# Kernel tuning notes

Hardware: AMD Instinct MI355X
Metric: run time of the kernel (lower is better)

## Reference

```python
import jax, jax.numpy as jnp
import numpy as np

N, T = 1024, 32
D_FEAT, GATE_START, GATE_END = 158, 158, 221
D_MODEL = 256
T_NHEAD, S_NHEAD = 4, 2
BETA = 5.0
LN_EPS = 1e-5


def _ln(x, g, b):
    mu = jnp.mean(x, axis=-1, keepdims=True)
    var = jnp.mean(jnp.square(x - mu), axis=-1, keepdims=True)
    return (x - mu) * jax.lax.rsqrt(var + LN_EPS) * g + b


def _pos_enc(t, d):
    pos = jnp.arange(t, dtype=jnp.float32)[:, None]
    div = jnp.exp(jnp.arange(0, d, 2, dtype=jnp.float32) * (-np.log(10000.0) / d))
    pe = jnp.zeros((t, d), dtype=jnp.float32)
    pe = pe.at[:, 0::2].set(jnp.sin(pos * div))
    pe = pe.at[:, 1::2].set(jnp.cos(pos * div))
    return pe


def _mha(xn, qw, kw, vw, nhead, temperature):
    # xn: [B, S, D] (already layer-normed); attention over axis S
    B, S, D = xn.shape
    dh = D // nhead
    q = (xn @ qw.T).reshape(B, S, nhead, dh)
    k = (xn @ kw.T).reshape(B, S, nhead, dh)
    v = (xn @ vw.T).reshape(B, S, nhead, dh)
    scores = jnp.einsum('bshd,bthd->bhst', q, k) / temperature
    a = jax.nn.softmax(scores, axis=-1)
    return jnp.einsum('bhst,bthd->bshd', a, v).reshape(B, S, D)


def _block(x, qw, kw, vw, n1g, n1b, n2g, n2b, f1w, f1b, f2w, f2b, nhead, temperature):
    xn = _ln(x, n1g, n1b)
    xt = xn + _mha(xn, qw, kw, vw, nhead, temperature)
    xt = _ln(xt, n2g, n2b)
    ffn = jnp.maximum(xt @ f1w.T + f1b, 0.0) @ f2w.T + f2b
    return xt + ffn


def _forward(x, gate_w, gate_b, proj_w, proj_b,
             tq, tk, tv, tn1g, tn1b, tn2g, tn2b, tf1w, tf1b, tf2w, tf2b,
             sq, sk, sv, sn1g, sn1b, sn2g, sn2b, sf1w, sf1b, sf2w, sf2b,
             temp_w, out_w, out_b):
    src = x[:, :, :GATE_START]                     # [N, T, d_feat]
    gate_in = x[:, -1, GATE_START:GATE_END]        # [N, d_gate]
    gate = D_FEAT * jax.nn.softmax((gate_in @ gate_w.T + gate_b) / BETA, axis=-1)
    src = src * gate[:, None, :]
    z = src @ proj_w.T + proj_b                    # [N, T, d_model]
    z = z + _pos_enc(z.shape[1], D_MODEL)
    # TAttention: attend over time, unscaled scores (temperature=1)
    z = _block(z, tq, tk, tv, tn1g, tn1b, tn2g, tn2b, tf1w, tf1b, tf2w, tf2b,
               T_NHEAD, 1.0)
    # SAttention: attend over stocks, temperature = sqrt(d_model/nhead)
    zs = _block(z.swapaxes(0, 1), sq, sk, sv, sn1g, sn1b, sn2g, sn2b,
                sf1w, sf1b, sf2w, sf2b, S_NHEAD, float(np.sqrt(D_MODEL / S_NHEAD)))
    z = zs.swapaxes(0, 1)                          # [N, T, d_model]
    # TemporalAttention pooling
    h = z @ temp_w.T
    lam = jax.nn.softmax(jnp.einsum('ntd,nd->nt', h, h[:, -1, :]), axis=1)
    pooled = jnp.einsum('nt,ntd->nd', lam, z)
    return (pooled @ out_w.T + out_b).squeeze(-1)  # [N]


def setup_inputs() -> dict:
    key = jax.random.key(0)
    ks = iter(jax.random.split(key, 32))
    s = 0.02
    d, f, g = D_MODEL, D_FEAT, GATE_END - GATE_START
    inp = {
        'x': jax.random.normal(next(ks), (N, T, GATE_END), dtype=jnp.float32),
        'gate_w': jax.random.normal(next(ks), (f, g)) * s,
        'gate_b': jnp.zeros((f,)),
        'proj_w': jax.random.normal(next(ks), (d, f)) * s,
        'proj_b': jnp.zeros((d,)),
        'tq': jax.random.normal(next(ks), (d, d)) * s,
        'tk': jax.random.normal(next(ks), (d, d)) * s,
        'tv': jax.random.normal(next(ks), (d, d)) * s,
        'tn1g': jnp.ones((d,)), 'tn1b': jnp.zeros((d,)),
        'tn2g': jnp.ones((d,)), 'tn2b': jnp.zeros((d,)),
        'tf1w': jax.random.normal(next(ks), (d, d)) * s, 'tf1b': jnp.zeros((d,)),
        'tf2w': jax.random.normal(next(ks), (d, d)) * s, 'tf2b': jnp.zeros((d,)),
        'sq': jax.random.normal(next(ks), (d, d)) * s,
        'sk': jax.random.normal(next(ks), (d, d)) * s,
        'sv': jax.random.normal(next(ks), (d, d)) * s,
        'sn1g': jnp.ones((d,)), 'sn1b': jnp.zeros((d,)),
        'sn2g': jnp.ones((d,)), 'sn2b': jnp.zeros((d,)),
        'sf1w': jax.random.normal(next(ks), (d, d)) * s, 'sf1b': jnp.zeros((d,)),
        'sf2w': jax.random.normal(next(ks), (d, d)) * s, 'sf2b': jnp.zeros((d,)),
        'temp_w': jax.random.normal(next(ks), (d, d)) * s,
        'out_w': jax.random.normal(next(ks), (1, d)) * s,
        'out_b': jnp.zeros((1,)),
    }
    return {k: v.astype(jnp.float32) for k, v in inp.items()}


def reference(x, gate_w, gate_b, proj_w, proj_b,
              tq, tk, tv, tn1g, tn1b, tn2g, tn2b, tf1w, tf1b, tf2w, tf2b,
              sq, sk, sv, sn1g, sn1b, sn2g, sn2b, sf1w, sf1b, sf2w, sf2b,
              temp_w, out_w, out_b):
    return _forward(x, gate_w, gate_b, proj_w, proj_b,
                    tq, tk, tv, tn1g, tn1b, tn2g, tn2b, tf1w, tf1b, tf2w, tf2b,
                    sq, sk, sv, sn1g, sn1b, sn2g, sn2b, sf1w, sf1b, sf2w, sf2b,
                    temp_w, out_w, out_b)
```

## Files before the change

### kernel.cpp

```cpp
#include <hip/hip_runtime.h>
#include <math.h>

#define NB   1024
#define TSEQ 32
#define DM   256
#define DF   158
#define GDIM 63
#define XROW 221

typedef unsigned short u16;
typedef __attribute__((ext_vector_type(8))) __bf16 bf16x8;
typedef __attribute__((ext_vector_type(4))) float f32x4;
#define MFMA16(a,b,c) __builtin_amdgcn_mfma_f32_16x16x32_bf16(a,b,c,0,0,0)

#define MODE_PROJ 0
#define MODE_QKVT 1
#define MODE_QKVS 2
#define MODE_TEMP 3

__device__ __forceinline__ u16 f2bf(float f){
  union { float f; unsigned int u; } c; c.f = f;
  unsigned int u = c.u;
  u += 0x7fffu + ((u >> 16) & 1u);
  return (u16)(u >> 16);
}

__device__ __forceinline__ u16 f2bf_t(float f){
  union { float f; unsigned int u; } c; c.f = f;
  return (u16)(c.u >> 16);
}

__device__ __forceinline__ void gl2lds16(const u16* g, u16* lds_wave_base, int lane){
#if __has_builtin(__builtin_amdgcn_global_load_lds)
  __builtin_amdgcn_global_load_lds(
      (const __attribute__((address_space(1))) unsigned int*)g,
      (__attribute__((address_space(3))) unsigned int*)lds_wave_base,
      16, 0, 0);
#else
  *reinterpret_cast<uint4*>(lds_wave_base + lane * 8) =
      *reinterpret_cast<const uint4*>(g);
#endif
}

__device__ __forceinline__ void ln_rows32(float* buf, int stride,
                                          const float* __restrict__ g,
                                          const float* __restrict__ b,
                                          int tid)
{
  const int s = tid >> 3, j = tid & 7;
  float* row = buf + s * stride;
  float sum = 0.f, sq = 0.f;
  #pragma unroll
  for (int k = 0; k < DM; k += 8){
    float v = row[k + j];
    sum += v; sq += v * v;
  }
  #pragma unroll
  for (int o = 1; o < 8; o <<= 1){
    sum += __shfl_xor(sum, o);
    sq  += __shfl_xor(sq, o);
  }
  const float mu  = sum * (1.f / DM);
  const float var = sq * (1.f / DM) - mu * mu;
  const float rs  = rsqrtf(var + 1e-5f);
  #pragma unroll
  for (int k = 0; k < DM; k += 8){
    float v = row[k + j];
    row[k + j] = (v - mu) * rs * g[k + j] + b[k + j];
  }
}

#define WB_TOT 770048

__global__ __launch_bounds__(256) void kConvAll(
    const float* __restrict__ tq, const float* __restrict__ tk, const float* __restrict__ tv,
    const float* __restrict__ sq, const float* __restrict__ sk, const float* __restrict__ sv,
    const float* __restrict__ tf1, const float* __restrict__ tf2,
    const float* __restrict__ sf1, const float* __restrict__ sf2,
    const float* __restrict__ tw, const float* __restrict__ pw,
    u16* __restrict__ WB)
{
  int i = blockIdx.x * 256 + threadIdx.x;
  if (i >= WB_TOT) return;
  if (i < 720896){
    int j = i >> 16, o = i & 65535;
    const float* s;
    switch (j){
      case 0: s = tq; break;  case 1: s = tk; break;  case 2: s = tv; break;
      case 3: s = sq; break;  case 4: s = sk; break;  case 5: s = sv; break;
      case 6: s = tf1; break; case 7: s = tf2; break;
      case 8: s = sf1; break; case 9: s = sf2; break;
      default: s = tw; break;
    }
    WB[i] = f2bf(s[o]);
  } else {
    int k = i - 720896;
    int row = k / 192, col = k - row * 192;
    WB[i] = (col < DF) ? f2bf(pw[row * DF + col]) : (u16)0;
  }
}


__global__ __launch_bounds__(256) void kGateSrc(
    const float* __restrict__ x,
    const float* __restrict__ gate_w, const float* __restrict__ gate_b,
    u16* __restrict__ SRC)
{
  __shared__ float s_gate[DF];
  __shared__ float s_gi[GDIM];
  const int tid = threadIdx.x;
  const int n = blockIdx.x;

  if (tid < GDIM) s_gi[tid] = x[(n * TSEQ + (TSEQ - 1)) * XROW + DF + tid];
  __syncthreads();
  float logit = 0.f;
  if (tid < DF){
    logit = gate_b[tid];
    const float* __restrict__ wr = gate_w + tid * GDIM;
    for (int g = 0; g < GDIM; ++g) logit += s_gi[g] * wr[g];
    logit *= 0.2f;
    s_gate[tid] = logit;
  }
  __syncthreads();
  {
    float mx = -1e30f;
    for (int f = 0; f < DF; ++f) mx = fmaxf(mx, s_gate[f]);
    float sm = 0.f;
    for (int f = 0; f < DF; ++f) sm += __expf(s_gate[f] - mx);
    __syncthreads();
    if (tid < DF) s_gate[tid] = (float)DF * __expf(logit - mx) / sm;
  }
  __syncthreads();

  for (int e = tid; e < TSEQ * 192; e += 256){
    int t = e / 192, f = e - t * 192;
    float v = 0.f;
    if (f < DF) v = x[(n * TSEQ + t) * XROW + f] * s_gate[f];
    SRC[(size_t)(n * TSEQ + t) * 192 + f] = f2bf(v);
  }
}


__global__ __launch_bounds__(256) void gemm_bf16(
    const u16* __restrict__ A, const u16* __restrict__ B,
    const int K, const int mode,
    const float* __restrict__ bias,
    float* __restrict__ outf,
    u16* __restrict__ ob0, u16* __restrict__ ob1, u16* __restrict__ ob2)
{
  __shared__ alignas(16) u16 sA[128 * 64];
  __shared__ alignas(16) u16 sB[128 * 64];
  const int tid = threadIdx.x;
  const int wv = tid >> 6, lane = tid & 63;
  const int wr = wv >> 1, wc = wv & 1;
  const int quad = lane >> 4, lc = lane & 15;
  const int n0 = blockIdx.y * 128;
  const bool tmaj = (mode == MODE_QKVS);
  const int tt = tmaj ? (blockIdx.x & 31) : 0;
  const int nb = tmaj ? (blockIdx.x >> 5) : 0;
  const int m0 = tmaj ? 0 : blockIdx.x * 128;

  f32x4 acc[4][4];
  #pragma unroll
  for (int i = 0; i < 4; ++i)
    #pragma unroll
    for (int j = 0; j < 4; ++j) acc[i][j] = (f32x4){0.f,0.f,0.f,0.f};

  for (int kt = 0; kt < K; kt += 64){
    __syncthreads();
    #pragma unroll
    for (int j = 0; j < 4; ++j){
      int c = wv * 64 + lane + j * 256;
      int row = c >> 3, blk = c & 7;
      int arow = tmaj ? ((nb * 128 + row) * 32 + tt) : (m0 + row);
      gl2lds16(A + (size_t)arow * K + kt + ((blk ^ (row & 7)) * 8),
               &sA[(wv * 64 + j * 256) * 8], lane);
      gl2lds16(B + (size_t)(n0 + row) * K + kt + ((blk ^ (row & 7)) * 8),
               &sB[(wv * 64 + j * 256) * 8], lane);
    }
    __syncthreads();
    #pragma unroll
    for (int kc = 0; kc < 2; ++kc){
      const int sw = ((kc * 4 + quad) ^ (lc & 7)) * 8;
      bf16x8 a[4], b[4];
      #pragma unroll
      for (int i = 0; i < 4; ++i){
        a[i] = *reinterpret_cast<const bf16x8*>(&sA[(wr * 64 + i * 16 + lc) * 64 + sw]);
        b[i] = *reinterpret_cast<const bf16x8*>(&sB[(wc * 64 + i * 16 + lc) * 64 + sw]);
      }
      #pragma unroll
      for (int i = 0; i < 4; ++i)
        #pragma unroll
        for (int j = 0; j < 4; ++j)
          acc[i][j] = MFMA16(a[i], b[j], acc[i][j]);
    }
  }

  const int rb = wr * 64 + quad * 4;
  const int cb = wc * 64 + lc;

  if (mode == MODE_PROJ){
    #pragma unroll
    for (int i = 0; i < 4; ++i)
      #pragma unroll
      for (int r = 0; r < 4; ++r){
        int row = m0 + rb + i * 16 + r;
        float ft = (float)(row & 31);
        #pragma unroll
        for (int j = 0; j < 4; ++j){
          int col = n0 + cb + j * 16;
          float div = __expf((float)(col & ~1) * -0.035977892f);
          float ang = ft * div;
          float pe = (col & 1) ? __cosf(ang) : __sinf(ang);
          outf[(size_t)row * 256 + col] = acc[i][j][r] + bias[col] + pe;
        }
      }
  } else if (mode == MODE_QKVT){
    #pragma unroll
    for (int i = 0; i < 4; ++i)
      #pragma unroll
      for (int r = 0; r < 4; ++r){
        int row = m0 + rb + i * 16 + r;
        #pragma unroll
        for (int j = 0; j < 4; ++j){
          int col = n0 + cb + j * 16;
          int sel = col >> 8, c = col & 255;
          u16 v = f2bf(acc[i][j][r]);
          if (sel == 0)      ob0[(size_t)row * 256 + c] = v;
          else if (sel == 1) ob1[(size_t)row * 256 + c] = v;
          else {
            int h = c >> 6, dd = c & 63;
            ob2[(((size_t)(row >> 5) * 4 + h) * 64 + dd) * 32 + (row & 31)] = v;
          }
        }
      }
  } else if (mode == MODE_QKVS){
    #pragma unroll
    for (int i = 0; i < 4; ++i)
      #pragma unroll
      for (int r = 0; r < 4; ++r){
        int rl = rb + i * 16 + r;
        int n = nb * 128 + rl;
        #pragma unroll
        for (int j = 0; j < 4; ++j){
          int col = n0 + cb + j * 16;
          int sel = col >> 8, c = col & 255;
          u16 v = f2bf(acc[i][j][r]);
          if (sel == 0)      ob0[((size_t)tt * NB + n) * 256 + c] = v;
          else if (sel == 1) ob1[((size_t)tt * NB + n) * 256 + c] = v;
          else {
            int h = c >> 7, dd = c & 127;
            ob2[(((size_t)tt * 2 + h) * 128 + dd) * NB + n] = v;
          }
        }
      }
  } else {
    #pragma unroll
    for (int i = 0; i < 4; ++i)
      #pragma unroll
      for (int r = 0; r < 4; ++r){
        int row = m0 + rb + i * 16 + r;
        #pragma unroll
        for (int j = 0; j < 4; ++j){
          int col = n0 + cb + j * 16;
          outf[(size_t)row * 256 + col] = acc[i][j][r];
        }
      }
  }
}


__global__ __launch_bounds__(256) void kLN(
    const float* __restrict__ X, const float* __restrict__ g,
    const float* __restrict__ b,
    u16* __restrict__ Xb, float* __restrict__ Xf)
{
  __shared__ float s_z[32 * DM];
  const int tid = threadIdx.x;
  const size_t base = (size_t)blockIdx.x * (32 * DM);
  for (int e = tid; e < 32 * DM; e += 256) s_z[e] = X[base + e];
  __syncthreads();
  ln_rows32(s_z, DM, g, b, tid);
  __syncthreads();
  for (int e = tid; e < 32 * DM; e += 256){
    float v = s_z[e];
    Xb[base + e] = f2bf(v);
    Xf[base + e] = v;
  }
}


__global__ __launch_bounds__(512) void kFFN(
    const float* __restrict__ X,
    const float* __restrict__ lg, const float* __restrict__ lb,
    const u16* __restrict__ w1, const float* __restrict__ b1,
    const u16* __restrict__ w2, const float* __restrict__ b2,
    float* __restrict__ outf, u16* __restrict__ obdual)
{
  __shared__ alignas(16) u16 sAB[24576];
  __shared__ alignas(16) u16 s_h1[128 * 256];
  __shared__ float s_mu[128], s_rs[128];
  __shared__ float s_lg[256], s_lb[256], s_b1[256], s_b2[256];

  const int tid = threadIdx.x;
  const int wv = tid >> 6, lane = tid & 63;
  const int quad = lane >> 4, lc = lane & 15;
  const int m0 = blockIdx.x * 128;
  const int m0w = (wv >> 1) * 32;
  const int n0w = (wv & 1) * 128;
  u16* sA = sAB;
  u16* sB = sAB + 8192;

  if (tid < 256){
    s_lg[tid] = lg[tid]; s_lb[tid] = lb[tid];
    s_b1[tid] = b1[tid]; s_b2[tid] = b2[tid];
  }

  {
    const int row = tid >> 2, j = tid & 3;
    const float4* xr = reinterpret_cast<const float4*>(X + (size_t)(m0 + row) * 256);
    float sum = 0.f, sq = 0.f;
    #pragma unroll
    for (int k = 0; k < 16; ++k){
      float4 v = xr[j + 4 * k];
      sum += v.x + v.y + v.z + v.w;
      sq  += v.x*v.x + v.y*v.y + v.z*v.z + v.w*v.w;
    }
    sum += __shfl_xor(sum, 1); sq += __shfl_xor(sq, 1);
    sum += __shfl_xor(sum, 2); sq += __shfl_xor(sq, 2);
    if (j == 0){
      float mu = sum * (1.f / 256.f);
      s_mu[row] = mu;
      s_rs[row] = rsqrtf(sq * (1.f / 256.f) - mu * mu + 1e-5f);
    }
  }
  __syncthreads();

  f32x4 acc[2][8];
  #pragma unroll
  for (int mt = 0; mt < 2; ++mt)
    #pragma unroll
    for (int j = 0; j < 8; ++j) acc[mt][j] = (f32x4){0.f,0.f,0.f,0.f};

  for (int kt = 0; kt < 4; ++kt){
    __syncthreads();
    {
      const int row = tid >> 2, c0 = (tid & 3) * 16;
      const float mu = s_mu[row], rs = s_rs[row];
      const float* xp = X + (size_t)(m0 + row) * 256 + kt * 64 + c0;
      u16 v16[16];
      #pragma unroll
      for (int k = 0; k < 4; ++k){
        float4 v = *reinterpret_cast<const float4*>(xp + 4 * k);
        int col = kt * 64 + c0 + 4 * k;
        v16[4*k+0] = f2bf((v.x - mu) * rs * s_lg[col+0] + s_lb[col+0]);
        v16[4*k+1] = f2bf((v.y - mu) * rs * s_lg[col+1] + s_lb[col+1]);
        v16[4*k+2] = f2bf((v.z - mu) * rs * s_lg[col+2] + s_lb[col+2]);
        v16[4*k+3] = f2bf((v.w - mu) * rs * s_lg[col+3] + s_lb[col+3]);
      }
      int b0 = c0 >> 3;
      *reinterpret_cast<uint4*>(&sA[row * 64 + ((b0    ) ^ (row & 7)) * 8]) = *reinterpret_cast<uint4*>(&v16[0]);
      *reinterpret_cast<uint4*>(&sA[row * 64 + ((b0 + 1) ^ (row & 7)) * 8]) = *reinterpret_cast<uint4*>(&v16[8]);
    }
    #pragma unroll
    for (int i = 0; i < 4; ++i){
      int c = tid + i * 512;
      int row = c >> 3, blk = c & 7;
      *reinterpret_cast<uint4*>(&sB[row * 64 + (blk ^ (row & 7)) * 8]) =
        *reinterpret_cast<const uint4*>(w1 + (size_t)row * 256 + kt * 64 + blk * 8);
    }
    __syncthreads();
    #pragma unroll
    for (int kc = 0; kc < 2; ++kc){
      const int sw = ((kc * 4 + quad) ^ (lc & 7)) * 8;
      bf16x8 a[2], b[8];
      #pragma unroll
      for (int mt = 0; mt < 2; ++mt)
        a[mt] = *reinterpret_cast<const bf16x8*>(&sA[(m0w + mt * 16 + lc) * 64 + sw]);
      #pragma unroll
      for (int j = 0; j < 8; ++j)
        b[j] = *reinterpret_cast<const bf16x8*>(&sB[(n0w + j * 16 + lc) * 64 + sw]);
      #pragma unroll
      for (int mt = 0; mt < 2; ++mt)
        #pragma unroll
        for (int j = 0; j < 8; ++j)
          acc[mt][j] = MFMA16(a[mt], b[j], acc[mt][j]);
    }
  }
  __syncthreads();

  #pragma unroll
  for (int mt = 0; mt < 2; ++mt)
    #pragma unroll
    for (int r = 0; r < 4; ++r){
      int row = m0w + mt * 16 + quad * 4 + r;
      #pragma unroll
      for (int j = 0; j < 8; ++j){
        int col = n0w + j * 16 + lc;
        u16 v = f2bf(fmaxf(acc[mt][j][r] + s_b1[col], 0.f));
        s_h1[row * 256 + (((col >> 3) ^ (row & 31)) << 3) + (col & 7)] = v;
      }
    }

  #pragma unroll
  for (int mt = 0; mt < 2; ++mt)
    #pragma unroll
    for (int j = 0; j < 8; ++j) acc[mt][j] = (f32x4){0.f,0.f,0.f,0.f};

  for (int kt = 0; kt < 4; ++kt){
    __syncthreads();
    #pragma unroll
    for (int i = 0; i < 4; ++i){
      int c = tid + i * 512;
      int row = c >> 3, blk = c & 7;
      *reinterpret_cast<uint4*>(&sAB[row * 64 + (blk ^ (row & 7)) * 8]) =
        *reinterpret_cast<const uint4*>(w2 + (size_t)row * 256 + kt * 64 + blk * 8);
    }
    __syncthreads();
    #pragma unroll
    for (int kc = 0; kc < 2; ++kc){
      const int sw = ((kc * 4 + quad) ^ (lc & 7)) * 8;
      bf16x8 a[2], b[8];
      #pragma unroll
      for (int mt = 0; mt < 2; ++mt){
        int row = m0w + mt * 16 + lc;
        int cb = kt * 8 + kc * 4 + quad;
        a[mt] = *reinterpret_cast<const bf16x8*>(
            &s_h1[row * 256 + ((cb ^ (row & 31)) << 3)]);
      }
      #pragma unroll
      for (int j = 0; j < 8; ++j)
        b[j] = *reinterpret_cast<const bf16x8*>(&sAB[(n0w + j * 16 + lc) * 64 + sw]);
      #pragma unroll
      for (int mt = 0; mt < 2; ++mt)
        #pragma unroll
        for (int j = 0; j < 8; ++j)
          acc[mt][j] = MFMA16(a[mt], b[j], acc[mt][j]);
    }
  }

  #pragma unroll
  for (int mt = 0; mt < 2; ++mt)
    #pragma unroll
    for (int r = 0; r < 4; ++r){
      int rowl = m0w + mt * 16 + quad * 4 + r;
      const float mu = s_mu[rowl], rs = s_rs[rowl];
      size_t base = (size_t)(m0 + rowl) * 256;
      #pragma unroll
      for (int j = 0; j < 8; ++j){
        int col = n0w + j * 16 + lc;
        float xn = (X[base + col] - mu) * rs * s_lg[col] + s_lb[col];
        float v = acc[mt][j][r] + s_b2[col] + xn;
        outf[base + col] = v;
        if (obdual) obdual[base + col] = f2bf(v);
      }
    }
}


__global__ __launch_bounds__(256) void kAttnT(
    const u16* __restrict__ Qt, const u16* __restrict__ Kt,
    const u16* __restrict__ VtT, const float* __restrict__ XN1f,
    float* __restrict__ X2)
{
  __shared__ alignas(16) u16 sQ[4][32 * 72];
  __shared__ alignas(16) u16 sK[4][32 * 72];
  __shared__ alignas(16) u16 sV[4][64 * 40];
  __shared__ alignas(16) u16 sP[4][32 * 40];

  const int tid = threadIdx.x;
  const int wv = tid >> 6, lane = tid & 63;
  const int quad = lane >> 4, lc = lane & 15;
  const int n = blockIdx.x;
  const int h = wv;
  const f32x4 zero4 = {0.f, 0.f, 0.f, 0.f};

  #pragma unroll
  for (int i = 0; i < 4; ++i){
    int c = lane + 64 * i;
    int row = c >> 3, blk = c & 7;
    *reinterpret_cast<uint4*>(&sQ[wv][row * 72 + blk * 8]) =
      *reinterpret_cast<const uint4*>(&Qt[((size_t)n * 32 + row) * 256 + h * 64 + blk * 8]);
    *reinterpret_cast<uint4*>(&sK[wv][row * 72 + blk * 8]) =
      *reinterpret_cast<const uint4*>(&Kt[((size_t)n * 32 + row) * 256 + h * 64 + blk * 8]);
    int rv = c >> 2, bv = c & 3;
    *reinterpret_cast<uint4*>(&sV[wv][rv * 40 + bv * 8]) =
      *reinterpret_cast<const uint4*>(&VtT[(((size_t)n * 4 + h) * 64 + rv) * 32 + bv * 8]);
  }
  __syncthreads();

  f32x4 s[2][2];
  #pragma unroll
  for (int mt = 0; mt < 2; ++mt)
    #pragma unroll
    for (int ct = 0; ct < 2; ++ct) s[mt][ct] = zero4;
  #pragma unroll
  for (int kc = 0; kc < 2; ++kc){
    bf16x8 aq[2], bk[2];
    #pragma unroll
    for (int mt = 0; mt < 2; ++mt)
      aq[mt] = *reinterpret_cast<const bf16x8*>(&sQ[wv][(mt * 16 + lc) * 72 + kc * 32 + quad * 8]);
    #pragma unroll
    for (int ct = 0; ct < 2; ++ct)
      bk[ct] = *reinterpret_cast<const bf16x8*>(&sK[wv][(ct * 16 + lc) * 72 + kc * 32 + quad * 8]);
    #pragma unroll
    for (int mt = 0; mt < 2; ++mt)
      #pragma unroll
      for (int ct = 0; ct < 2; ++ct)
        s[mt][ct] = MFMA16(aq[mt], bk[ct], s[mt][ct]);
  }

  #pragma unroll
  for (int mt = 0; mt < 2; ++mt){
    #pragma unroll
    for (int r = 0; r < 4; ++r){
      float v0 = s[mt][0][r], v1 = s[mt][1][r];
      float mx = fmaxf(v0, v1);
      #pragma unroll
      for (int msk = 1; msk < 16; msk <<= 1) mx = fmaxf(mx, __shfl_xor(mx, msk));
      float p0 = __expf(v0 - mx), p1 = __expf(v1 - mx);
      float sm = p0 + p1;
      #pragma unroll
      for (int msk = 1; msk < 16; msk <<= 1) sm += __shfl_xor(sm, msk);
      float inv = 1.f / sm;
      sP[wv][(mt * 16 + quad * 4 + r) * 40 + lc]      = f2bf(p0 * inv);
      sP[wv][(mt * 16 + quad * 4 + r) * 40 + lc + 16] = f2bf(p1 * inv);
    }
  }
  __syncthreads();

  #pragma unroll
  for (int mt = 0; mt < 2; ++mt){
    bf16x8 ap = *reinterpret_cast<const bf16x8*>(&sP[wv][(mt * 16 + lc) * 40 + quad * 8]);
    #pragma unroll
    for (int ct = 0; ct < 4; ++ct){
      bf16x8 bv = *reinterpret_cast<const bf16x8*>(&sV[wv][(ct * 16 + lc) * 40 + quad * 8]);
      f32x4 o = MFMA16(ap, bv, zero4);
      #pragma unroll
      for (int r = 0; r < 4; ++r){
        int t = mt * 16 + quad * 4 + r;
        size_t idx = ((size_t)n * 32 + t) * 256 + h * 64 + ct * 16 + lc;
        X2[idx] = XN1f[idx] + o[r];
      }
    }
  }
}


__global__ __launch_bounds__(512) void kB2_flash_mfma(
    const u16* __restrict__ Qh, const u16* __restrict__ Kh,
    const u16* __restrict__ VT, const float* __restrict__ XNs,
    float* __restrict__ XT)
{
  __shared__ alignas(16) u16 smem[28160];
  u16* s_k  = smem;
  u16* s_vt = smem + 8704;
  u16* s_p  = smem + 17920;

  const int tid = threadIdx.x;
  const int wv = tid >> 6, lane = tid & 63;
  const int wq = wv & 3, wk = wv >> 2;
  const int quad = lane >> 4, lc = lane & 15;
  const int t = blockIdx.x >> 1, h = blockIdx.x & 1;
  const int n0 = blockIdx.y * 128;
  const float c_exp2 = 0.12752887f;
  const int qb = n0 + wq * 32;

  bf16x8 qf[2][4];
  #pragma unroll
  for (int mt = 0; mt < 2; ++mt){
    const u16* qp = Qh + ((size_t)(t * NB + qb + mt * 16 + lc)) * DM + h * 128 + quad * 8;
    #pragma unroll
    for (int kc = 0; kc < 4; ++kc)
      qf[mt][kc] = *reinterpret_cast<const bf16x8*>(qp + kc * 32);
  }

  f32x4 o[2][8];
  #pragma unroll
  for (int mt = 0; mt < 2; ++mt)
    #pragma unroll
    for (int f = 0; f < 8; ++f) o[mt][f] = (f32x4){0.f, 0.f, 0.f, 0.f};
  float l_acc[2][4] = {{0.f,0.f,0.f,0.f},{0.f,0.f,0.f,0.f}};

  const u16* kbase  = Kh + (size_t)t * NB * DM + h * 128;
  const u16* vtbase = VT + (size_t)(t * 2 + h) * 128 * NB;
  u16* pw = s_p + wv * 1280;

  for (int j0 = 0; j0 < NB; j0 += 64){
    __syncthreads();
    #pragma unroll
    for (int it = 0; it < 2; ++it){
      int c = tid + it * 512;
      int row = c >> 4, part = c & 15;
      *reinterpret_cast<uint4*>(&s_k[row * 136 + part * 8]) =
        *reinterpret_cast<const uint4*>(kbase + (size_t)(j0 + row) * DM + part * 8);
      int rv = c >> 3, pv = c & 7;
      *reinterpret_cast<uint4*>(&s_vt[rv * 72 + pv * 8]) =
        *reinterpret_cast<const uint4*>(vtbase + (size_t)rv * NB + j0 + pv * 8);
    }
    __syncthreads();

    f32x4 s[2][2];
    #pragma unroll
    for (int mt = 0; mt < 2; ++mt)
      #pragma unroll
      for (int nt = 0; nt < 2; ++nt) s[mt][nt] = (f32x4){0.f,0.f,0.f,0.f};
    #pragma unroll
    for (int kc = 0; kc < 4; ++kc){
      #pragma unroll
      for (int nt = 0; nt < 2; ++nt){
        bf16x8 bk = *reinterpret_cast<const bf16x8*>(
            &s_k[(lc + 16 * nt + 32 * wk) * 136 + kc * 32 + quad * 8]);
        #pragma unroll
        for (int mt = 0; mt < 2; ++mt)
          s[mt][nt] = MFMA16(qf[mt][kc], bk, s[mt][nt]);
      }
    }

    #pragma unroll
    for (int mt = 0; mt < 2; ++mt)
      #pragma unroll
      for (int nt = 0; nt < 2; ++nt)
        #pragma unroll
        for (int r = 0; r < 4; ++r){
          float p = exp2f(s[mt][nt][r] * c_exp2);
          l_acc[mt][r] += p;
          pw[(mt * 16 + quad * 4 + r) * 40 + lc + 16 * nt] = f2bf_t(p);
        }

    bf16x8 ap[2];
    #pragma unroll
    for (int mt = 0; mt < 2; ++mt)
      ap[mt] = *reinterpret_cast<const bf16x8*>(&pw[(mt * 16 + lc) * 40 + quad * 8]);
    #pragma unroll
    for (int f = 0; f < 8; ++f){
      bf16x8 bv = *reinterpret_cast<const bf16x8*>(
          &s_vt[(lc + 16 * f) * 72 + 32 * wk + quad * 8]);
      #pragma unroll
      for (int mt = 0; mt < 2; ++mt)
        o[mt][f] = MFMA16(ap[mt], bv, o[mt][f]);
    }
  }

  float* fo = (float*)smem;
  float* fl = (float*)smem + 8192;

  __syncthreads();
  if (wk == 1){
    int base = (wq * 64 + lane) * 32;
    #pragma unroll
    for (int f = 0; f < 8; ++f)
      #pragma unroll
      for (int r = 0; r < 4; ++r) fo[base + f * 4 + r] = o[0][f][r];
    int lb = (wq * 64 + lane) * 8;
    #pragma unroll
    for (int mt = 0; mt < 2; ++mt)
      #pragma unroll
      for (int r = 0; r < 4; ++r) fl[lb + mt * 4 + r] = l_acc[mt][r];
  }
  __syncthreads();
  if (wk == 0){
    int base = (wq * 64 + lane) * 32;
    #pragma unroll
    for (int f = 0; f < 8; ++f)
      #pragma unroll
      for (int r = 0; r < 4; ++r) o[0][f][r] += fo[base + f * 4 + r];
    int lb = (wq * 64 + lane) * 8;
    #pragma unroll
    for (int mt = 0; mt < 2; ++mt)
      #pragma unroll
      for (int r = 0; r < 4; ++r){
        l_acc[mt][r] += fl[lb + mt * 4 + r];
        #pragma unroll
        for (int msk = 1; msk < 16; msk <<= 1)
          l_acc[mt][r] += __shfl_xor(l_acc[mt][r], msk);
      }
    #pragma unroll
    for (int r = 0; r < 4; ++r){
      float linv = 1.f / l_acc[0][r];
      int row = qb + quad * 4 + r;
      size_t xnb = ((size_t)row * TSEQ + t) * DM + h * 128 + lc;
      size_t xtb = ((size_t)t * NB + row) * DM + h * 128 + lc;
      #pragma unroll
      for (int f = 0; f < 8; ++f)
        XT[xtb + f * 16] = XNs[xnb + f * 16] + o[0][f][r] * linv;
    }
  }
  __syncthreads();
  if (wk == 1){
    int base = (wq * 64 + lane) * 32;
    #pragma unroll
    for (int f = 0; f < 8; ++f)
      #pragma unroll
      for (int r = 0; r < 4; ++r) fo[base + f * 4 + r] = o[1][f][r];
  }
  __syncthreads();
  if (wk == 0){
    int base = (wq * 64 + lane) * 32;
    #pragma unroll
    for (int f = 0; f < 8; ++f)
      #pragma unroll
      for (int r = 0; r < 4; ++r) o[1][f][r] += fo[base + f * 4 + r];
    #pragma unroll
    for (int r = 0; r < 4; ++r){
      float linv = 1.f / l_acc[1][r];
      int row = qb + 16 + quad * 4 + r;
      size_t xnb = ((size_t)row * TSEQ + t) * DM + h * 128 + lc;
      size_t xtb = ((size_t)t * NB + row) * DM + h * 128 + lc;
      #pragma unroll
      for (int f = 0; f < 8; ++f)
        XT[xtb + f * 16] = XNs[xnb + f * 16] + o[1][f][r] * linv;
    }
  }
}


__global__ __launch_bounds__(256) void kC_pool(
    const float* __restrict__ Ht, const float* __restrict__ ZS,
    const float* __restrict__ out_w, const float* __restrict__ out_b,
    float* __restrict__ out)
{
  __shared__ float s_z[32 * DM];
  __shared__ float s_h[32 * 260];
  __shared__ float s_sc[32];
  __shared__ float s_red[4];
  const int tid = threadIdx.x;
  const int n = blockIdx.x;

  for (int e = tid; e < 32 * DM; e += 256){
    int i = e >> 8, dd = e & 255;
    s_h[i * 260 + dd] = Ht[((size_t)i * NB + n) * DM + dd];
    s_z[e]            = ZS[((size_t)i * NB + n) * DM + dd];
  }
  __syncthreads();

  {
    const int s = tid >> 3, j = tid & 7;
    float acc = 0.f;
    #pragma unroll
    for (int k = 0; k < DM; k += 8) acc += s_h[s * 260 + k + j] * s_h[31 * 260 + k + j];
    #pragma unroll
    for (int o = 1; o < 8; o <<= 1) acc += __shfl_xor(acc, o);
    if (j == 0) s_sc[s] = acc;
  }
  __syncthreads();

  float mx = -1e30f;
  #pragma unroll
  for (int s = 0; s < 32; ++s) mx = fmaxf(mx, s_sc[s]);
  float sm = 0.f;
  #pragma unroll
  for (int s = 0; s < 32; ++s) sm += __expf(s_sc[s] - mx);
  const float inv = 1.f / sm;

  const int d = tid;
  float pooled = 0.f;
  #pragma unroll
  for (int s = 0; s < 32; ++s) pooled += __expf(s_sc[s] - mx) * inv * s_z[s * DM + d];

  float val = pooled * out_w[d];
  #pragma unroll
  for (int o = 1; o < 64; o <<= 1) val += __shfl_xor(val, o);
  if ((tid & 63) == 0) s_red[tid >> 6] = val;
  __syncthreads();
  if (tid == 0) out[n] = s_red[0] + s_red[1] + s_red[2] + s_red[3] + out_b[0];
}


extern "C" void kernel_launch(void* const* d_in, const int* in_sizes, int n_in,
                              void* d_out, int out_size, void* d_ws, size_t ws_size,
                              hipStream_t stream)
{
  const float* x      = (const float*)d_in[0];
  const float* gate_w = (const float*)d_in[1];
  const float* gate_b = (const float*)d_in[2];
  const float* proj_w = (const float*)d_in[3];
  const float* proj_b = (const float*)d_in[4];
  const float* tq   = (const float*)d_in[5];
  const float* tk   = (const float*)d_in[6];
  const float* tv   = (const float*)d_in[7];
  const float* tn1g = (const float*)d_in[8];
  const float* tn1b = (const float*)d_in[9];
  const float* tn2g = (const float*)d_in[10];
  const float* tn2b = (const float*)d_in[11];
  const float* tf1w = (const float*)d_in[12];
  const float* tf1b = (const float*)d_in[13];
  const float* tf2w = (const float*)d_in[14];
  const float* tf2b = (const float*)d_in[15];
  const float* sq   = (const float*)d_in[16];
  const float* sk   = (const float*)d_in[17];
  const float* sv   = (const float*)d_in[18];
  const float* sn1g = (const float*)d_in[19];
  const float* sn1b = (const float*)d_in[20];
  const float* sn2g = (const float*)d_in[21];
  const float* sn2b = (const float*)d_in[22];
  const float* sf1w = (const float*)d_in[23];
  const float* sf1b = (const float*)d_in[24];
  const float* sf2w = (const float*)d_in[25];
  const float* sf2b = (const float*)d_in[26];
  const float* temp_w = (const float*)d_in[27];
  const float* out_w  = (const float*)d_in[28];
  const float* out_b  = (const float*)d_in[29];

  float* W = (float*)d_ws;
  const size_t F = (size_t)NB * TSEQ * DM;

  float* Z  = W;
  float* XF = W + F;
  u16* U0 = (u16*)(W + 2 * F);
  u16* U1 = (u16*)(W + 2 * F) + F;
  u16* U2 = (u16*)(W + 3 * F);
  u16* U3 = (u16*)(W + 3 * F) + F;
  u16* SRC = (u16*)(W + 4 * F);
  u16* WB  = (u16*)(W + 4 * F + 3145728 + 4096);

  kConvAll<<<(WB_TOT + 255) / 256, 256, 0, stream>>>(
      tq, tk, tv, sq, sk, sv, tf1w, tf2w, sf1w, sf2w, temp_w, proj_w, WB);
  kGateSrc<<<NB, 256, 0, stream>>>(x, gate_w, gate_b, SRC);
  gemm_bf16<<<dim3(256, 2), 256, 0, stream>>>(SRC, WB + 720896, 192, MODE_PROJ,
      proj_b, Z, nullptr, nullptr, nullptr);
  kLN<<<NB, 256, 0, stream>>>(Z, tn1g, tn1b, U0, XF);
  gemm_bf16<<<dim3(256, 6), 256, 0, stream>>>(U0, WB, 256, MODE_QKVT,
      nullptr, nullptr, U1, U2, U3);
  kAttnT<<<NB, 256, 0, stream>>>(U1, U2, U3, XF, Z);
  kFFN<<<256, 512, 0, stream>>>(Z, tn2g, tn2b, WB + 393216, tf1b,
      WB + 458752, tf2b, Z, nullptr);
  kLN<<<NB, 256, 0, stream>>>(Z, sn1g, sn1b, U2, XF);
  gemm_bf16<<<dim3(256, 6), 256, 0, stream>>>(U2, WB + 196608, 256, MODE_QKVS,
      nullptr, nullptr, U3, U1, U0);
  kB2_flash_mfma<<<dim3(64, 8), 512, 0, stream>>>(U3, U1, U0, XF, Z);
  kFFN<<<256, 512, 0, stream>>>(Z, sn2g, sn2b, WB + 524288, sf1b,
      WB + 589824, sf2b, Z, U0);
  gemm_bf16<<<dim3(256, 2), 256, 0, stream>>>(U0, WB + 655360, 256, MODE_TEMP,
      nullptr, XF, nullptr, nullptr, nullptr);
  kC_pool<<<NB, 256, 0, stream>>>(XF, Z, out_w, out_b, (float*)d_out);
}
```

Before: 478.8 us.

## Widen GEMM tiles to 128x256 with 512 threads; async swizzled LDS loads in flash attention

The bf16 GEMM now uses 8 waves per block and a 256-wide N tile, so each A tile is loaded once per two former blocks and the grid halves. The stock-attention flash kernel replaces padded register-staged K/V copies with direct global-to-LDS loads into XOR-swizzled unpadded layouts, with matching read indexing. The aim is to cut redundant A traffic, register staging and LDS padding. The cost is fewer blocks per GEMM launch (256 for proj/temp) and more LDS per block, which may lower occupancy.

```diff
diff --git a/kernel.cpp b/kernel.cpp
--- a/kernel.cpp
+++ b/kernel.cpp
@@ -141,7 +141,7 @@
 }
 
 
-__global__ __launch_bounds__(256) void gemm_bf16(
+__global__ __launch_bounds__(512) void gemm_bf16(
     const u16* __restrict__ A, const u16* __restrict__ B,
     const int K, const int mode,
     const float* __restrict__ bias,
@@ -149,12 +149,12 @@
     u16* __restrict__ ob0, u16* __restrict__ ob1, u16* __restrict__ ob2)
 {
   __shared__ alignas(16) u16 sA[128 * 64];
-  __shared__ alignas(16) u16 sB[128 * 64];
+  __shared__ alignas(16) u16 sB[256 * 64];
   const int tid = threadIdx.x;
   const int wv = tid >> 6, lane = tid & 63;
-  const int wr = wv >> 1, wc = wv & 1;
+  const int wr = wv >> 2, wc = wv & 3;
   const int quad = lane >> 4, lc = lane & 15;
-  const int n0 = blockIdx.y * 128;
+  const int n0 = blockIdx.y * 256;
   const bool tmaj = (mode == MODE_QKVS);
   const int tt = tmaj ? (blockIdx.x & 31) : 0;
   const int nb = tmaj ? (blockIdx.x >> 5) : 0;
@@ -169,14 +169,19 @@
   for (int kt = 0; kt < K; kt += 64){
     __syncthreads();
     #pragma unroll
-    for (int j = 0; j < 4; ++j){
-      int c = wv * 64 + lane + j * 256;
-      int row = c >> 3, blk = c & 7;
+    for (int j = 0; j < 2; ++j){
+      int cA = wv * 2 + j;
+      int row = cA * 8 + (lane >> 3), blk = lane & 7;
       int arow = tmaj ? ((nb * 128 + row) * 32 + tt) : (m0 + row);
       gl2lds16(A + (size_t)arow * K + kt + ((blk ^ (row & 7)) * 8),
-               &sA[(wv * 64 + j * 256) * 8], lane);
+               &sA[cA * 512], lane);
+    }
+    #pragma unroll
+    for (int j = 0; j < 4; ++j){
+      int cB = wv * 4 + j;
+      int row = cB * 8 + (lane >> 3), blk = lane & 7;
       gl2lds16(B + (size_t)(n0 + row) * K + kt + ((blk ^ (row & 7)) * 8),
-               &sB[(wv * 64 + j * 256) * 8], lane);
+               &sB[cB * 512], lane);
     }
     __syncthreads();
     #pragma unroll
@@ -552,10 +557,10 @@
     const u16* __restrict__ VT, const float* __restrict__ XNs,
     float* __restrict__ XT)
 {
-  __shared__ alignas(16) u16 smem[28160];
+  __shared__ alignas(16) u16 smem[26624];
   u16* s_k  = smem;
-  u16* s_vt = smem + 8704;
-  u16* s_p  = smem + 17920;
+  u16* s_vt = smem + 8192;
+  u16* s_p  = smem + 16384;
 
   const int tid = threadIdx.x;
   const int wv = tid >> 6, lane = tid & 63;
@@ -589,14 +594,15 @@
   for (int j0 = 0; j0 < NB; j0 += 64){
     __syncthreads();
     #pragma unroll
-    for (int it = 0; it < 2; ++it){
-      int c = tid + it * 512;
-      int row = c >> 4, part = c & 15;
-      *reinterpret_cast<uint4*>(&s_k[row * 136 + part * 8]) =
-        *reinterpret_cast<const uint4*>(kbase + (size_t)(j0 + row) * DM + part * 8);
-      int rv = c >> 3, pv = c & 7;
-      *reinterpret_cast<uint4*>(&s_vt[rv * 72 + pv * 8]) =
-        *reinterpret_cast<const uint4*>(vtbase + (size_t)rv * NB + j0 + pv * 8);
+    for (int i = 0; i < 2; ++i){
+      int row = wv * 8 + i * 4 + (lane >> 4);
+      int blk = lane & 15;
+      gl2lds16(kbase + (size_t)(j0 + row) * DM + ((blk ^ (row & 15)) * 8),
+               s_k + wv * 1024 + i * 512, lane);
+      int rv = wv * 16 + i * 8 + (lane >> 3);
+      int pv = lane & 7;
+      gl2lds16(vtbase + (size_t)rv * NB + j0 + ((pv ^ (rv & 7)) * 8),
+               s_vt + wv * 1024 + i * 512, lane);
     }
     __syncthreads();
 
@@ -609,8 +615,9 @@
     for (int kc = 0; kc < 4; ++kc){
       #pragma unroll
       for (int nt = 0; nt < 2; ++nt){
+        int krow = lc + 16 * nt + 32 * wk;
         bf16x8 bk = *reinterpret_cast<const bf16x8*>(
-            &s_k[(lc + 16 * nt + 32 * wk) * 136 + kc * 32 + quad * 8]);
+            &s_k[krow * 128 + (((kc * 4 + quad) ^ lc) * 8)]);
         #pragma unroll
         for (int mt = 0; mt < 2; ++mt)
           s[mt][nt] = MFMA16(qf[mt][kc], bk, s[mt][nt]);
@@ -634,8 +641,9 @@
       ap[mt] = *reinterpret_cast<const bf16x8*>(&pw[(mt * 16 + lc) * 40 + quad * 8]);
     #pragma unroll
     for (int f = 0; f < 8; ++f){
+      int vrow = lc + 16 * f;
       bf16x8 bv = *reinterpret_cast<const bf16x8*>(
-          &s_vt[(lc + 16 * f) * 72 + 32 * wk + quad * 8]);
+          &s_vt[vrow * 64 + (((4 * wk + quad) ^ (lc & 7)) * 8)]);
       #pragma unroll
       for (int mt = 0; mt < 2; ++mt)
         o[mt][f] = MFMA16(ap[mt], bv, o[mt][f]);
@@ -817,21 +825,21 @@
   kConvAll<<<(WB_TOT + 255) / 256, 256, 0, stream>>>(
       tq, tk, tv, sq, sk, sv, tf1w, tf2w, sf1w, sf2w, temp_w, proj_w, WB);
   kGateSrc<<<NB, 256, 0, stream>>>(x, gate_w, gate_b, SRC);
-  gemm_bf16<<<dim3(256, 2), 256, 0, stream>>>(SRC, WB + 720896, 192, MODE_PROJ,
+  gemm_bf16<<<dim3(256, 1), 512, 0, stream>>>(SRC, WB + 720896, 192, MODE_PROJ,
       proj_b, Z, nullptr, nullptr, nullptr);
   kLN<<<NB, 256, 0, stream>>>(Z, tn1g, tn1b, U0, XF);
-  gemm_bf16<<<dim3(256, 6), 256, 0, stream>>>(U0, WB, 256, MODE_QKVT,
+  gemm_bf16<<<dim3(256, 3), 512, 0, stream>>>(U0, WB, 256, MODE_QKVT,
       nullptr, nullptr, U1, U2, U3);
   kAttnT<<<NB, 256, 0, stream>>>(U1, U2, U3, XF, Z);
   kFFN<<<256, 512, 0, stream>>>(Z, tn2g, tn2b, WB + 393216, tf1b,
       WB + 458752, tf2b, Z, nullptr);
   kLN<<<NB, 256, 0, stream>>>(Z, sn1g, sn1b, U2, XF);
-  gemm_bf16<<<dim3(256, 6), 256, 0, stream>>>(U2, WB + 196608, 256, MODE_QKVS,
+  gemm_bf16<<<dim3(256, 3), 512, 0, stream>>>(U2, WB + 196608, 256, MODE_QKVS,
       nullptr, nullptr, U3, U1, U0);
   kB2_flash_mfma<<<dim3(64, 8), 512, 0, stream>>>(U3, U1, U0, XF, Z);
   kFFN<<<256, 512, 0, stream>>>(Z, sn2g, sn2b, WB + 524288, sf1b,
       WB + 589824, sf2b, Z, U0);
-  gemm_bf16<<<dim3(256, 2), 256, 0, stream>>>(U0, WB + 655360, 256, MODE_TEMP,
+  gemm_bf16<<<dim3(256, 1), 512, 0, stream>>>(U0, WB + 655360, 256, MODE_TEMP,
       nullptr, XF, nullptr, nullptr, nullptr);
   kC_pool<<<NB, 256, 0, stream>>>(XF, Z, out_w, out_b, (float*)d_out);
 }
```

New measurement: 551.9 us. 1.15x slower.

## Fuse LayerNorms into projection GEMM and temporal FFN epilogue

Applied to the files above, without the earlier changes.

Replaces the projection GEMM plus separate LN kernel with a single kProjLN kernel that computes the full 256-wide row per block and applies positional encoding, bias and LayerNorm in the epilogue. The temporal FFN epilogue also applies the spatial block's first LayerNorm directly, writing the normalized fp32 and bf16 outputs. This removes two LN launches and their full-tensor fp32 global round trips, at the cost of cross-wave reductions through shared memory and a projection launch with half as many blocks.

```diff
diff --git a/kernel.cpp b/kernel.cpp
--- a/kernel.cpp
+++ b/kernel.cpp
@@ -13,7 +13,6 @@
 typedef __attribute__((ext_vector_type(4))) float f32x4;
 #define MFMA16(a,b,c) __builtin_amdgcn_mfma_f32_16x16x32_bf16(a,b,c,0,0,0)
 
-#define MODE_PROJ 0
 #define MODE_QKVT 1
 #define MODE_QKVS 2
 #define MODE_TEMP 3
@@ -40,34 +39,6 @@
   *reinterpret_cast<uint4*>(lds_wave_base + lane * 8) =
       *reinterpret_cast<const uint4*>(g);
 #endif
-}
-
-__device__ __forceinline__ void ln_rows32(float* buf, int stride,
-                                          const float* __restrict__ g,
-                                          const float* __restrict__ b,
-                                          int tid)
-{
-  const int s = tid >> 3, j = tid & 7;
-  float* row = buf + s * stride;
-  float sum = 0.f, sq = 0.f;
-  #pragma unroll
-  for (int k = 0; k < DM; k += 8){
-    float v = row[k + j];
-    sum += v; sq += v * v;
-  }
-  #pragma unroll
-  for (int o = 1; o < 8; o <<= 1){
-    sum += __shfl_xor(sum, o);
-    sq  += __shfl_xor(sq, o);
-  }
-  const float mu  = sum * (1.f / DM);
-  const float var = sq * (1.f / DM) - mu * mu;
-  const float rs  = rsqrtf(var + 1e-5f);
-  #pragma unroll
-  for (int k = 0; k < DM; k += 8){
-    float v = row[k + j];
-    row[k + j] = (v - mu) * rs * g[k + j] + b[k + j];
-  }
 }
 
 #define WB_TOT 770048
@@ -141,10 +112,116 @@
 }
 
 
+__global__ __launch_bounds__(512) void kProjLN(
+    const u16* __restrict__ SRC, const u16* __restrict__ Bw,
+    const float* __restrict__ bias,
+    const float* __restrict__ lg, const float* __restrict__ lb,
+    u16* __restrict__ Xb, float* __restrict__ Xf)
+{
+  __shared__ alignas(16) u16 sA[128 * 64];
+  __shared__ alignas(16) u16 sB[256 * 64];
+  __shared__ float s_sum[4 * 128], s_sq[4 * 128];
+  __shared__ float s_lg[256], s_lb[256], s_bias[256];
+
+  const int tid = threadIdx.x;
+  const int wv = tid >> 6, lane = tid & 63;
+  const int wr = wv >> 2, wc = wv & 3;
+  const int quad = lane >> 4, lc = lane & 15;
+  const int m0 = blockIdx.x * 128;
+
+  if (tid < 256){ s_lg[tid] = lg[tid]; s_lb[tid] = lb[tid]; s_bias[tid] = bias[tid]; }
+
+  f32x4 acc[4][4];
+  #pragma unroll
+  for (int i = 0; i < 4; ++i)
+    #pragma unroll
+    for (int j = 0; j < 4; ++j) acc[i][j] = (f32x4){0.f,0.f,0.f,0.f};
+
+  for (int kt = 0; kt < 192; kt += 64){
+    __syncthreads();
+    #pragma unroll
+    for (int i = 0; i < 2; ++i){
+      int c = tid + i * 512;
+      int row = c >> 3, blk = c & 7;
+      *reinterpret_cast<uint4*>(&sA[row * 64 + ((blk ^ (row & 7)) * 8)]) =
+        *reinterpret_cast<const uint4*>(SRC + (size_t)(m0 + row) * 192 + kt + blk * 8);
+    }
+    #pragma unroll
+    for (int i = 0; i < 4; ++i){
+      int c = tid + i * 512;
+      int row = c >> 3, blk = c & 7;
+      *reinterpret_cast<uint4*>(&sB[row * 64 + ((blk ^ (row & 7)) * 8)]) =
+        *reinterpret_cast<const uint4*>(Bw + (size_t)row * 192 + kt + blk * 8);
+    }
+    __syncthreads();
+    #pragma unroll
+    for (int kc = 0; kc < 2; ++kc){
+      const int sw = ((kc * 4 + quad) ^ (lc & 7)) * 8;
+      bf16x8 a[4], b[4];
+      #pragma unroll
+      for (int i = 0; i < 4; ++i){
+        a[i] = *reinterpret_cast<const bf16x8*>(&sA[(wr * 64 + i * 16 + lc) * 64 + sw]);
+        b[i] = *reinterpret_cast<const bf16x8*>(&sB[(wc * 64 + i * 16 + lc) * 64 + sw]);
+      }
+      #pragma unroll
+      for (int i = 0; i < 4; ++i)
+        #pragma unroll
+        for (int j = 0; j < 4; ++j)
+          acc[i][j] = MFMA16(a[i], b[j], acc[i][j]);
+    }
+  }
+
+  const int rb = wr * 64 + quad * 4;
+  #pragma unroll
+  for (int i = 0; i < 4; ++i)
+    #pragma unroll
+    for (int r = 0; r < 4; ++r){
+      int rowl = rb + i * 16 + r;
+      float ft = (float)((m0 + rowl) & 31);
+      float ps = 0.f, pq = 0.f;
+      #pragma unroll
+      for (int j = 0; j < 4; ++j){
+        int col = wc * 64 + j * 16 + lc;
+        float div = __expf((float)(col & ~1) * -0.035977892f);
+        float ang = ft * div;
+        float pe = (col & 1) ? __cosf(ang) : __sinf(ang);
+        float v = acc[i][j][r] + s_bias[col] + pe;
+        acc[i][j][r] = v;
+        ps += v; pq += v * v;
+      }
+      #pragma unroll
+      for (int msk = 1; msk < 16; msk <<= 1){
+        ps += __shfl_xor(ps, msk);
+        pq += __shfl_xor(pq, msk);
+      }
+      if (lc == 0){ s_sum[wc * 128 + rowl] = ps; s_sq[wc * 128 + rowl] = pq; }
+    }
+  __syncthreads();
+
+  #pragma unroll
+  for (int i = 0; i < 4; ++i)
+    #pragma unroll
+    for (int r = 0; r < 4; ++r){
+      int rowl = rb + i * 16 + r;
+      float sum = s_sum[rowl] + s_sum[128 + rowl] + s_sum[256 + rowl] + s_sum[384 + rowl];
+      float sq  = s_sq[rowl]  + s_sq[128 + rowl]  + s_sq[256 + rowl]  + s_sq[384 + rowl];
+      float mu = sum * (1.f / 256.f);
+      float rs = rsqrtf(sq * (1.f / 256.f) - mu * mu + 1e-5f);
+      size_t base = (size_t)(m0 + rowl) * 256;
+      #pragma unroll
+      for (int j = 0; j < 4; ++j){
+        int col = wc * 64 + j * 16 + lc;
+        float xn = (acc[i][j][r] - mu) * rs * s_lg[col] + s_lb[col];
+        Xf[base + col] = xn;
+        Xb[base + col] = f2bf(xn);
+      }
+    }
+}
+
+
 __global__ __launch_bounds__(256) void gemm_bf16(
     const u16* __restrict__ A, const u16* __restrict__ B,
     const int K, const int mode,
-    const float* __restrict__ bias,
     float* __restrict__ outf,
     u16* __restrict__ ob0, u16* __restrict__ ob1, u16* __restrict__ ob2)
 {
@@ -199,23 +276,7 @@
   const int rb = wr * 64 + quad * 4;
   const int cb = wc * 64 + lc;
 
-  if (mode == MODE_PROJ){
-    #pragma unroll
-    for (int i = 0; i < 4; ++i)
-      #pragma unroll
-      for (int r = 0; r < 4; ++r){
-        int row = m0 + rb + i * 16 + r;
-        float ft = (float)(row & 31);
-        #pragma unroll
-        for (int j = 0; j < 4; ++j){
-          int col = n0 + cb + j * 16;
-          float div = __expf((float)(col & ~1) * -0.035977892f);
-          float ang = ft * div;
-          float pe = (col & 1) ? __cosf(ang) : __sinf(ang);
-          outf[(size_t)row * 256 + col] = acc[i][j][r] + bias[col] + pe;
-        }
-      }
-  } else if (mode == MODE_QKVT){
+  if (mode == MODE_QKVT){
     #pragma unroll
     for (int i = 0; i < 4; ++i)
       #pragma unroll
@@ -270,37 +331,20 @@
 }
 
 
-__global__ __launch_bounds__(256) void kLN(
-    const float* __restrict__ X, const float* __restrict__ g,
-    const float* __restrict__ b,
-    u16* __restrict__ Xb, float* __restrict__ Xf)
-{
-  __shared__ float s_z[32 * DM];
-  const int tid = threadIdx.x;
-  const size_t base = (size_t)blockIdx.x * (32 * DM);
-  for (int e = tid; e < 32 * DM; e += 256) s_z[e] = X[base + e];
-  __syncthreads();
-  ln_rows32(s_z, DM, g, b, tid);
-  __syncthreads();
-  for (int e = tid; e < 32 * DM; e += 256){
-    float v = s_z[e];
-    Xb[base + e] = f2bf(v);
-    Xf[base + e] = v;
-  }
-}
-
-
 __global__ __launch_bounds__(512) void kFFN(
     const float* __restrict__ X,
     const float* __restrict__ lg, const float* __restrict__ lb,
     const u16* __restrict__ w1, const float* __restrict__ b1,
     const u16* __restrict__ w2, const float* __restrict__ b2,
+    const float* __restrict__ og, const float* __restrict__ ob,
     float* __restrict__ outf, u16* __restrict__ obdual)
 {
   __shared__ alignas(16) u16 sAB[24576];
   __shared__ alignas(16) u16 s_h1[128 * 256];
   __shared__ float s_mu[128], s_rs[128];
   __shared__ float s_lg[256], s_lb[256], s_b1[256], s_b2[256];
+  __shared__ float s_og[256], s_ob[256];
+  __shared__ float s_os[2 * 128], s_oq[2 * 128];
 
   const int tid = threadIdx.x;
   const int wv = tid >> 6, lane = tid & 63;
@@ -314,6 +358,7 @@
   if (tid < 256){
     s_lg[tid] = lg[tid]; s_lb[tid] = lb[tid];
     s_b1[tid] = b1[tid]; s_b2[tid] = b2[tid];
+    if (og){ s_og[tid] = og[tid]; s_ob[tid] = ob[tid]; }
   }
 
   {
@@ -439,22 +484,70 @@
     }
   }
 
-  #pragma unroll
-  for (int mt = 0; mt < 2; ++mt)
-    #pragma unroll
-    for (int r = 0; r < 4; ++r){
-      int rowl = m0w + mt * 16 + quad * 4 + r;
-      const float mu = s_mu[rowl], rs = s_rs[rowl];
-      size_t base = (size_t)(m0 + rowl) * 256;
-      #pragma unroll
-      for (int j = 0; j < 8; ++j){
-        int col = n0w + j * 16 + lc;
-        float xn = (X[base + col] - mu) * rs * s_lg[col] + s_lb[col];
-        float v = acc[mt][j][r] + s_b2[col] + xn;
-        outf[base + col] = v;
-        if (obdual) obdual[base + col] = f2bf(v);
-      }
-    }
+  if (og){
+    #pragma unroll
+    for (int mt = 0; mt < 2; ++mt)
+      #pragma unroll
+      for (int r = 0; r < 4; ++r){
+        int rowl = m0w + mt * 16 + quad * 4 + r;
+        const float mu = s_mu[rowl], rs = s_rs[rowl];
+        size_t base = (size_t)(m0 + rowl) * 256;
+        float ps = 0.f, pq = 0.f;
+        #pragma unroll
+        for (int j = 0; j < 8; ++j){
+          int col = n0w + j * 16 + lc;
+          float xn = (X[base + col] - mu) * rs * s_lg[col] + s_lb[col];
+          float v = acc[mt][j][r] + s_b2[col] + xn;
+          acc[mt][j][r] = v;
+          ps += v; pq += v * v;
+        }
+        #pragma unroll
+        for (int msk = 1; msk < 16; msk <<= 1){
+          ps += __shfl_xor(ps, msk);
+          pq += __shfl_xor(pq, msk);
+        }
+        if (lc == 0){
+          s_os[(wv & 1) * 128 + rowl] = ps;
+          s_oq[(wv & 1) * 128 + rowl] = pq;
+        }
+      }
+    __syncthreads();
+    #pragma unroll
+    for (int mt = 0; mt < 2; ++mt)
+      #pragma unroll
+      for (int r = 0; r < 4; ++r){
+        int rowl = m0w + mt * 16 + quad * 4 + r;
+        float sum = s_os[rowl] + s_os[128 + rowl];
+        float sq  = s_oq[rowl] + s_oq[128 + rowl];
+        float mu2 = sum * (1.f / 256.f);
+        float rs2 = rsqrtf(sq * (1.f / 256.f) - mu2 * mu2 + 1e-5f);
+        size_t base = (size_t)(m0 + rowl) * 256;
+        #pragma unroll
+        for (int j = 0; j < 8; ++j){
+          int col = n0w + j * 16 + lc;
+          float w = (acc[mt][j][r] - mu2) * rs2 * s_og[col] + s_ob[col];
+          outf[base + col] = w;
+          obdual[base + col] = f2bf(w);
+        }
+      }
+  } else {
+    #pragma unroll
+    for (int mt = 0; mt < 2; ++mt)
+      #pragma unroll
+      for (int r = 0; r < 4; ++r){
+        int rowl = m0w + mt * 16 + quad * 4 + r;
+        const float mu = s_mu[rowl], rs = s_rs[rowl];
+        size_t base = (size_t)(m0 + rowl) * 256;
+        #pragma unroll
+        for (int j = 0; j < 8; ++j){
+          int col = n0w + j * 16 + lc;
+          float xn = (X[base + col] - mu) * rs * s_lg[col] + s_lb[col];
+          float v = acc[mt][j][r] + s_b2[col] + xn;
+          outf[base + col] = v;
+          if (obdual) obdual[base + col] = f2bf(v);
+        }
+      }
+  }
 }
 
 
@@ -817,21 +910,18 @@
   kConvAll<<<(WB_TOT + 255) / 256, 256, 0, stream>>>(
       tq, tk, tv, sq, sk, sv, tf1w, tf2w, sf1w, sf2w, temp_w, proj_w, WB);
   kGateSrc<<<NB, 256, 0, stream>>>(x, gate_w, gate_b, SRC);
-  gemm_bf16<<<dim3(256, 2), 256, 0, stream>>>(SRC, WB + 720896, 192, MODE_PROJ,
-      proj_b, Z, nullptr, nullptr, nullptr);
-  kLN<<<NB, 256, 0, stream>>>(Z, tn1g, tn1b, U0, XF);
+  kProjLN<<<256, 512, 0, stream>>>(SRC, WB + 720896, proj_b, tn1g, tn1b, U0, XF);
   gemm_bf16<<<dim3(256, 6), 256, 0, stream>>>(U0, WB, 256, MODE_QKVT,
-      nullptr, nullptr, U1, U2, U3);
+      nullptr, U1, U2, U3);
   kAttnT<<<NB, 256, 0, stream>>>(U1, U2, U3, XF, Z);
   kFFN<<<256, 512, 0, stream>>>(Z, tn2g, tn2b, WB + 393216, tf1b,
-      WB + 458752, tf2b, Z, nullptr);
-  kLN<<<NB, 256, 0, stream>>>(Z, sn1g, sn1b, U2, XF);
+      WB + 458752, tf2b, sn1g, sn1b, XF, U2);
   gemm_bf16<<<dim3(256, 6), 256, 0, stream>>>(U2, WB + 196608, 256, MODE_QKVS,
-      nullptr, nullptr, U3, U1, U0);
+      nullptr, U3, U1, U0);
   kB2_flash_mfma<<<dim3(64, 8), 512, 0, stream>>>(U3, U1, U0, XF, Z);
   kFFN<<<256, 512, 0, stream>>>(Z, sn2g, sn2b, WB + 524288, sf1b,
-      WB + 589824, sf2b, Z, U0);
+      WB + 589824, sf2b, nullptr, nullptr, Z, U0);
   gemm_bf16<<<dim3(256, 2), 256, 0, stream>>>(U0, WB + 655360, 256, MODE_TEMP,
-      nullptr, XF, nullptr, nullptr, nullptr);
+      XF, nullptr, nullptr, nullptr);
   kC_pool<<<NB, 256, 0, stream>>>(XF, Z, out_w, out_b, (float*)d_out);
 }
```

After: 450.3 us. 1.06x faster.
